# Optimization experiments

Hardware: AMD Instinct MI355X
Metric: run time of the kernel (lower is better)

## Reference

```python
import jax, jax.numpy as jnp
import numpy as np
from functools import partial

K = 64
KERNEL_SIZE = 16
TAU = 10.0
THETA = 0.5
GAMMA = 10.0
ALPHA = float(np.exp(-1.0 / TAU))
BETA = 1.0 - ALPHA

@jax.custom_vjp
def spike(x):
    return (x >= 0).astype(x.dtype)

def _spike_fwd(x):
    return spike(x), x

def _spike_bwd(x, g):
    surrogate = GAMMA * jnp.maximum(1.0 - GAMMA * jnp.abs(x), 0.0)
    return (g * surrogate,)

spike.defvjp(_spike_fwd, _spike_bwd)

def setup_inputs() -> dict:
    key = jax.random.key(0)
    k1, k2 = jax.random.split(key)
    B, T = 256, 4096
    x = jax.random.normal(k1, (B, 1, T), dtype=jnp.float32)
    # conv weight [K, 1, ks], init N(0, 1/sqrt(ks))
    W = jax.random.normal(k2, (K, 1, KERNEL_SIZE), dtype=jnp.float32) / np.sqrt(KERNEL_SIZE)
    return {"x": x, "W": W}

def _forward(x, W):
    B = x.shape[0]
    x = x.reshape(B, 1, -1)  # [B,1,T]
    # causal conv: left pad ks-1 -> output length T
    u = jax.lax.conv_general_dilated(
        x, W,
        window_strides=(1,),
        padding=[(KERNEL_SIZE - 1, 0)],
        dimension_numbers=("NCH", "OIH", "NCH"),
    )  # [B,K,T]
    u_t = jnp.transpose(u, (2, 0, 1))  # [T,B,K]
    v0 = jnp.zeros((B, K), dtype=x.dtype)

    def step(v, ut):
        v = ALPHA * v + BETA * ut                      # leak + input
        s_raw = spike(v - THETA)                        # [B,K]
        winner = jax.lax.stop_gradient(jnp.argmax(v, axis=1))  # [B]
        winner_spiked = jnp.take_along_axis(s_raw, winner[:, None], axis=1)  # [B,1]
        wta_mask = jax.nn.one_hot(winner, K, dtype=s_raw.dtype) * winner_spiked
        s = s_raw * wta_mask
        v = v - s * THETA                               # reset
        return v, s

    _, spikes_t = jax.lax.scan(step, v0, u_t)  # [T,B,K]
    return jnp.transpose(spikes_t, (1, 2, 0))  # [B,K,T]

def reference(x, W):
    return _forward(x, W)
```

## Files before the change

kernel.cpp:

```cpp
#include <hip/hip_runtime.h>

#define T_LEN  4096
#define KS     16
#define NSEG   16
#define SEG_CH 16
#define WARM_CH 24

#define ALPHA_F 0.9048374180359595f
#define BETA_F  0.09516258196404048f
#define THETA_F 0.5f

typedef float f32x2 __attribute__((ext_vector_type(2)));

__device__ __forceinline__ f32x2 pk_mul(f32x2 a, f32x2 b) {
  f32x2 d;
  asm("v_pk_mul_f32 %0, %1, %2" : "=v"(d) : "v"(a), "v"(b));
  return d;
}
__device__ __forceinline__ f32x2 pk_fma(f32x2 a, f32x2 b, f32x2 c) {
  f32x2 d;
  asm("v_pk_fma_f32 %0, %1, %2, %3" : "=v"(d) : "v"(a), "v"(b), "v"(c));
  return d;
}

__device__ __forceinline__ float wave64_max_all(float v) {
  float m, t;
  asm("s_nop 1\n\t"
      "v_max_f32 %0, %2, %2 quad_perm:[1,0,3,2] row_mask:0xf bank_mask:0xf\n\t"
      "s_nop 1\n\t"
      "v_max_f32 %0, %0, %0 quad_perm:[2,3,0,1] row_mask:0xf bank_mask:0xf\n\t"
      "s_nop 1\n\t"
      "v_max_f32 %0, %0, %0 row_half_mirror row_mask:0xf bank_mask:0xf\n\t"
      "s_nop 1\n\t"
      "v_max_f32 %0, %0, %0 row_mirror row_mask:0xf bank_mask:0xf\n\t"
      "v_mov_b32 %1, %0\n\t"
      "s_nop 1\n\t"
      "v_permlane32_swap_b32 %1, %0\n\t"
      "s_nop 1\n\t"
      "v_max_f32 %0, %0, %1\n\t"
      "v_mov_b32 %1, %0\n\t"
      "s_nop 1\n\t"
      "v_permlane16_swap_b32 %1, %0\n\t"
      "s_nop 1\n\t"
      "v_max_f32 %0, %0, %1"
      : "=&v"(m), "=&v"(t)
      : "v"(v));
  return m;
}

__global__ __launch_bounds__(64, 4)
void convlif_wta_kernel(const float* __restrict__ x, const float* __restrict__ W,
                        float* __restrict__ out) {
  const int blk  = blockIdx.x;
  const int b    = blk >> 4;
  const int seg  = blk & (NSEG - 1);
  const int lane = threadIdx.x;

  const int cout0  = seg * SEG_CH;
  const int cstart = (cout0 > WARM_CH) ? (cout0 - WARM_CH) : 0;
  const int cend   = cout0 + SEG_CH;

  f32x2 wp[KS];
  {
    const float4* w4 = reinterpret_cast<const float4*>(W + lane * KS);
    #pragma unroll
    for (int q = 0; q < 4; ++q) {
      float4 a = w4[q];
      wp[4*q+0] = (f32x2){a.x, a.x}; wp[4*q+1] = (f32x2){a.y, a.y};
      wp[4*q+2] = (f32x2){a.z, a.z}; wp[4*q+3] = (f32x2){a.w, a.w};
    }
  }

  const float4* xv4 = reinterpret_cast<const float4*>(x + (size_t)b * T_LEN);
  float* orow = out + ((size_t)(b * 64 + lane)) * T_LEN;

  f32x2 a2[8];

  auto conv_chunk = [&](int c) {
    f32x2 xp[16];
    if (c == 0) {
      #pragma unroll
      for (int n = 0; n < 8; ++n) xp[n] = (f32x2){0.0f, 0.0f};
    } else {
      const int b4 = 4 * c - 4;
      #pragma unroll
      for (int q = 0; q < 4; ++q) {
        float4 a = xv4[b4 + q];
        xp[2*q+0] = (f32x2){a.x, a.y};
        xp[2*q+1] = (f32x2){a.z, a.w};
      }
    }
    #pragma unroll
    for (int q = 0; q < 4; ++q) {
      float4 a = xv4[4*c + q];
      xp[8+2*q+0] = (f32x2){a.x, a.y};
      xp[8+2*q+1] = (f32x2){a.z, a.w};
    }
    f32x2 yp[15];
    #pragma unroll
    for (int n = 0; n < 15; ++n) yp[n] = (f32x2){xp[n].y, xp[n+1].x};

    #pragma unroll
    for (int m = 0; m < 8; ++m) {
      f32x2 acc = pk_mul(wp[0], yp[m]);
      #pragma unroll
      for (int j = 1; j < KS; ++j)
        acc = pk_fma(wp[j], (j & 1) ? xp[m + (j+1)/2] : yp[m + j/2], acc);
      a2[m] = acc;
    }
  };

  float v = 0.0f;

  for (int c = cstart; c < cout0; ++c) {
    conv_chunk(c);
    #pragma unroll
    for (int i = 0; i < 16; ++i) {
      float ui = BETA_F * ((i & 1) ? a2[i >> 1].y : a2[i >> 1].x);
      float vr = fmaf(ALPHA_F, v, ui);
      float vm = vr - THETA_F;
      unsigned long long sp = __ballot(vr >= THETA_F);
      bool c1 = (vr >= THETA_F);
      v = c1 ? vm : vr;
      if (__builtin_expect((sp & (sp - 1ull)) != 0ull, 0)) {
        float m = wave64_max_all(vr);
        unsigned long long eq = __ballot(vr == m);
        bool win = (lane == __builtin_ctzll(eq));
        v = win ? vm : vr;
      }
    }
  }

  for (int c = cout0; c < cend; ++c) {
    conv_chunk(c);
    float sv[16];
    #pragma unroll
    for (int i = 0; i < 16; ++i) {
      float ui = BETA_F * ((i & 1) ? a2[i >> 1].y : a2[i >> 1].x);
      float vr = fmaf(ALPHA_F, v, ui);
      float vm = vr - THETA_F;
      unsigned long long sp = __ballot(vr >= THETA_F);
      bool c1 = (vr >= THETA_F);
      sv[i] = c1 ? 1.0f : 0.0f;
      v     = c1 ? vm : vr;
      if (__builtin_expect((sp & (sp - 1ull)) != 0ull, 0)) {
        float m = wave64_max_all(vr);
        unsigned long long eq = __ballot(vr == m);
        bool win = (lane == __builtin_ctzll(eq));
        sv[i] = win ? 1.0f : 0.0f;
        v     = win ? vm : vr;
      }
    }

    float4* p = reinterpret_cast<float4*>(orow + (size_t)c * 16);
    p[0] = make_float4(sv[0],  sv[1],  sv[2],  sv[3]);
    p[1] = make_float4(sv[4],  sv[5],  sv[6],  sv[7]);
    p[2] = make_float4(sv[8],  sv[9],  sv[10], sv[11]);
    p[3] = make_float4(sv[12], sv[13], sv[14], sv[15]);
  }
}

extern "C" void kernel_launch(void* const* d_in, const int* in_sizes, int n_in,
                              void* d_out, int out_size, void* d_ws, size_t ws_size,
                              hipStream_t stream) {
  const float* x   = (const float*)d_in[0];
  const float* W   = (const float*)d_in[1];
  float*       out = (float*)d_out;
  convlif_wta_kernel<<<dim3(256 * NSEG), dim3(64), 0, stream>>>(x, W, out);
}
```

Baseline: 130.0 us.

## Software-pipeline conv with LIF scan and halve segment count

```diff
diff --git a/kernel.cpp b/kernel.cpp
--- a/kernel.cpp
+++ b/kernel.cpp
@@ -2,26 +2,13 @@
 
 #define T_LEN  4096
 #define KS     16
-#define NSEG   16
-#define SEG_CH 16
+#define NSEG   8
+#define SEG_CH 32
 #define WARM_CH 24
 
 #define ALPHA_F 0.9048374180359595f
 #define BETA_F  0.09516258196404048f
 #define THETA_F 0.5f
-
-typedef float f32x2 __attribute__((ext_vector_type(2)));
-
-__device__ __forceinline__ f32x2 pk_mul(f32x2 a, f32x2 b) {
-  f32x2 d;
-  asm("v_pk_mul_f32 %0, %1, %2" : "=v"(d) : "v"(a), "v"(b));
-  return d;
-}
-__device__ __forceinline__ f32x2 pk_fma(f32x2 a, f32x2 b, f32x2 c) {
-  f32x2 d;
-  asm("v_pk_fma_f32 %0, %1, %2, %3" : "=v"(d) : "v"(a), "v"(b), "v"(c));
-  return d;
-}
 
 __device__ __forceinline__ float wave64_max_all(float v) {
   float m, t;
@@ -48,11 +35,11 @@
   return m;
 }
 
-__global__ __launch_bounds__(64, 4)
+__global__ __launch_bounds__(64, 2)
 void convlif_wta_kernel(const float* __restrict__ x, const float* __restrict__ W,
                         float* __restrict__ out) {
   const int blk  = blockIdx.x;
-  const int b    = blk >> 4;
+  const int b    = blk >> 3;
   const int seg  = blk & (NSEG - 1);
   const int lane = threadIdx.x;
 
@@ -60,64 +47,70 @@
   const int cstart = (cout0 > WARM_CH) ? (cout0 - WARM_CH) : 0;
   const int cend   = cout0 + SEG_CH;
 
-  f32x2 wp[KS];
+  float w[KS];
   {
     const float4* w4 = reinterpret_cast<const float4*>(W + lane * KS);
     #pragma unroll
     for (int q = 0; q < 4; ++q) {
       float4 a = w4[q];
-      wp[4*q+0] = (f32x2){a.x, a.x}; wp[4*q+1] = (f32x2){a.y, a.y};
-      wp[4*q+2] = (f32x2){a.z, a.z}; wp[4*q+3] = (f32x2){a.w, a.w};
+      w[4*q+0] = a.x; w[4*q+1] = a.y; w[4*q+2] = a.z; w[4*q+3] = a.w;
     }
   }
 
   const float4* xv4 = reinterpret_cast<const float4*>(x + (size_t)b * T_LEN);
   float* orow = out + ((size_t)(b * 64 + lane)) * T_LEN;
 
-  f32x2 a2[8];
+  float uA[16], uB[16];
+  float xwA[32], xwB[32];
 
-  auto conv_chunk = [&](int c) {
-    f32x2 xp[16];
-    if (c == 0) {
-      #pragma unroll
-      for (int n = 0; n < 8; ++n) xp[n] = (f32x2){0.0f, 0.0f};
-    } else {
-      const int b4 = 4 * c - 4;
-      #pragma unroll
-      for (int q = 0; q < 4; ++q) {
-        float4 a = xv4[b4 + q];
-        xp[2*q+0] = (f32x2){a.x, a.y};
-        xp[2*q+1] = (f32x2){a.z, a.w};
-      }
-    }
+  auto load_win = [&](float (&dst)[32], int k) {
+    const int b4 = 4 * k - 4;
     #pragma unroll
-    for (int q = 0; q < 4; ++q) {
-      float4 a = xv4[4*c + q];
-      xp[8+2*q+0] = (f32x2){a.x, a.y};
-      xp[8+2*q+1] = (f32x2){a.z, a.w};
-    }
-    f32x2 yp[15];
-    #pragma unroll
-    for (int n = 0; n < 15; ++n) yp[n] = (f32x2){xp[n].y, xp[n+1].x};
-
-    #pragma unroll
-    for (int m = 0; m < 8; ++m) {
-      f32x2 acc = pk_mul(wp[0], yp[m]);
-      #pragma unroll
-      for (int j = 1; j < KS; ++j)
-        acc = pk_fma(wp[j], (j & 1) ? xp[m + (j+1)/2] : yp[m + j/2], acc);
-      a2[m] = acc;
+    for (int q = 0; q < 8; ++q) {
+      float4 a = xv4[b4 + q];
+      dst[4*q+0] = a.x; dst[4*q+1] = a.y; dst[4*q+2] = a.z; dst[4*q+3] = a.w;
     }
   };
 
   float v = 0.0f;
 
-  for (int c = cstart; c < cout0; ++c) {
-    conv_chunk(c);
+  {
+    float xf0[32];
+    if (cstart == 0) {
+      #pragma unroll
+      for (int m = 0; m < 16; ++m) xf0[m] = 0.0f;
+      #pragma unroll
+      for (int q = 0; q < 4; ++q) {
+        float4 a = xv4[q];
+        xf0[16+4*q+0] = a.x; xf0[16+4*q+1] = a.y;
+        xf0[16+4*q+2] = a.z; xf0[16+4*q+3] = a.w;
+      }
+    } else {
+      load_win(xf0, cstart);
+    }
     #pragma unroll
     for (int i = 0; i < 16; ++i) {
-      float ui = BETA_F * ((i & 1) ? a2[i >> 1].y : a2[i >> 1].x);
-      float vr = fmaf(ALPHA_F, v, ui);
+      float acc = w[0] * xf0[1 + i];
+      #pragma unroll
+      for (int j = 1; j < KS; ++j) acc = fmaf(w[j], xf0[1 + i + j], acc);
+      uA[i] = BETA_F * acc;
+    }
+    load_win(xwA, cstart + 1);
+  }
+
+  auto fused_warm = [&](float (&cur)[16], float (&nxt)[16],
+                        float (&curw)[32], float (&nxtw)[32], int c) {
+    {
+      int k = c + 2; if (k > cend - 1) k = cend - 1;
+      load_win(nxtw, k);
+    }
+    #pragma unroll
+    for (int i = 0; i < 16; ++i) {
+      float acc = w[0] * curw[1 + i];
+      #pragma unroll
+      for (int j = 1; j < KS; ++j) acc = fmaf(w[j], curw[1 + i + j], acc);
+      nxt[i] = BETA_F * acc;
+      float vr = fmaf(ALPHA_F, v, cur[i]);
       float vm = vr - THETA_F;
       unsigned long long sp = __ballot(vr >= THETA_F);
       bool c1 = (vr >= THETA_F);
@@ -129,15 +122,23 @@
         v = win ? vm : vr;
       }
     }
-  }
+  };
 
-  for (int c = cout0; c < cend; ++c) {
-    conv_chunk(c);
+  auto fused_out = [&](float (&cur)[16], float (&nxt)[16],
+                       float (&curw)[32], float (&nxtw)[32], int c) {
+    {
+      int k = c + 2; if (k > cend - 1) k = cend - 1;
+      load_win(nxtw, k);
+    }
     float sv[16];
     #pragma unroll
     for (int i = 0; i < 16; ++i) {
-      float ui = BETA_F * ((i & 1) ? a2[i >> 1].y : a2[i >> 1].x);
-      float vr = fmaf(ALPHA_F, v, ui);
+      float acc = w[0] * curw[1 + i];
+      #pragma unroll
+      for (int j = 1; j < KS; ++j) acc = fmaf(w[j], curw[1 + i + j], acc);
+      nxt[i] = BETA_F * acc;
+
+      float vr = fmaf(ALPHA_F, v, cur[i]);
       float vm = vr - THETA_F;
       unsigned long long sp = __ballot(vr >= THETA_F);
       bool c1 = (vr >= THETA_F);
@@ -151,12 +152,20 @@
         v     = win ? vm : vr;
       }
     }
-
     float4* p = reinterpret_cast<float4*>(orow + (size_t)c * 16);
     p[0] = make_float4(sv[0],  sv[1],  sv[2],  sv[3]);
     p[1] = make_float4(sv[4],  sv[5],  sv[6],  sv[7]);
     p[2] = make_float4(sv[8],  sv[9],  sv[10], sv[11]);
     p[3] = make_float4(sv[12], sv[13], sv[14], sv[15]);
+  };
+
+  for (int c = cstart; c < cout0; c += 2) {
+    fused_warm(uA, uB, xwA, xwB, c);
+    fused_warm(uB, uA, xwB, xwA, c + 1);
+  }
+  for (int c = cout0; c < cend; c += 2) {
+    fused_out(uA, uB, xwA, xwB, c);
+    fused_out(uB, uA, xwB, xwA, c + 1);
   }
 }
 
```

New measurement: 123.5 us. 1.05x faster.
